# Optimization experiments

Hardware: AMD Instinct MI355X
Metric: run time of the kernel (lower is better)

The kernel has to match this reference:

```python
import jax, jax.numpy as jnp
import numpy as np

N = 30000
SLOPE = 0.2  # PyG GATConv default negative_slope


def _gat_conv(x, src, dst, W, a_src, a_dst, b, heads, out_ch, concat):
    """PyG GATConv (add_self_loops already applied), eval mode (no dropout).
    x: [N, F_in]; src/dst: [E] int; W: [F_in, heads*out_ch];
    a_src/a_dst: [heads, out_ch]; b: [heads*out_ch] or [out_ch]."""
    n = x.shape[0]
    h = (x @ W).reshape(n, heads, out_ch)              # [N, H, C]
    al_src = jnp.sum(h * a_src, axis=-1)               # [N, H]
    al_dst = jnp.sum(h * a_dst, axis=-1)               # [N, H]
    e = jax.nn.leaky_relu(al_src[src] + al_dst[dst], SLOPE)  # [E, H]
    # segment softmax over incoming edges of each destination node
    m = jax.ops.segment_max(e, dst, num_segments=n)
    ex = jnp.exp(e - m[dst])
    denom = jax.ops.segment_sum(ex, dst, num_segments=n)
    alpha = ex / (denom[dst] + 1e-16)                  # [E, H]
    msg = h[src] * alpha[..., None]                    # [E, H, C]
    out = jax.ops.segment_sum(msg, dst, num_segments=n)  # [N, H, C]
    out = out.reshape(n, heads * out_ch) if concat else out.mean(axis=1)
    return out + b


def setup_inputs() -> dict:
    key = jax.random.key(0)
    ks = jax.random.split(key, 20)
    E = 480000
    IN, H0, H1, LAT = 256, 64, 128, 32
    HEADS = 4
    x = jax.random.normal(ks[0], (N, IN), dtype=jnp.float32)
    edge_index = jax.random.randint(ks[1], (2, E), 0, N, dtype=jnp.int32)

    def gp(k, fin, heads, outc, concat):
        k1, k2, k3, k4 = jax.random.split(k, 4)
        s = 0.1
        W = jax.random.normal(k1, (fin, heads * outc), dtype=jnp.float32) * s
        a_s = jax.random.normal(k2, (heads, outc), dtype=jnp.float32) * s
        a_d = jax.random.normal(k3, (heads, outc), dtype=jnp.float32) * s
        b = jax.random.normal(k4, (heads * outc if concat else outc,), dtype=jnp.float32) * s
        return W, a_s, a_d, b

    W1, as1, ad1, b1 = gp(ks[2], IN, HEADS, H0, True)
    W2, as2, ad2, b2 = gp(ks[3], H0 * HEADS, HEADS, H1, True)
    Wm, asm, adm, bm = gp(ks[4], H1 * HEADS, HEADS, LAT, False)
    Wl, asl, adl, bl = gp(ks[5], H1 * HEADS, HEADS, LAT, False)
    return dict(x=x, edge_index=edge_index,
                W1=W1, as1=as1, ad1=ad1, b1=b1,
                W2=W2, as2=as2, ad2=ad2, b2=b2,
                Wm=Wm, asm=asm, adm=adm, bm=bm,
                Wl=Wl, asl=asl, adl=adl, bl=bl)


def reference(x, edge_index, W1, as1, ad1, b1, W2, as2, ad2, b2,
              Wm, asm, adm, bm, Wl, asl, adl, bl):
    n = x.shape[0]
    # add self loops (PyG GATConv default)
    loop = jnp.arange(n, dtype=edge_index.dtype)
    src = jnp.concatenate([edge_index[0], loop])
    dst = jnp.concatenate([edge_index[1], loop])

    out = _gat_conv(x, src, dst, W1, as1, ad1, b1, heads=4, out_ch=64, concat=True)
    out = jax.nn.relu(out)
    out = _gat_conv(out, src, dst, W2, as2, ad2, b2, heads=4, out_ch=128, concat=True)
    out = jax.nn.relu(out)
    # F.dropout with training=False (eval) is identity
    z_mean = _gat_conv(out, src, dst, Wm, asm, adm, bm, heads=4, out_ch=32, concat=False)
    z_logstd = _gat_conv(out, src, dst, Wl, asl, adl, bl, heads=4, out_ch=32, concat=False)
    return z_mean, z_logstd
```

## Files before the change

### kernel.cpp

```cpp
#include <hip/hip_runtime.h>
#include <cstddef>

typedef __attribute__((ext_vector_type(8))) short short8;
typedef __attribute__((ext_vector_type(4))) float f32x4;
typedef __attribute__((ext_vector_type(8))) _Float16 half8;
typedef __attribute__((ext_vector_type(4))) _Float16 half4;

__device__ __forceinline__ unsigned short f2h(float f) {
    union { _Float16 h; unsigned short u; } x; x.h = (_Float16)f; return x.u;
}
__device__ __forceinline__ float lrelu(float v) { return v > 0.f ? v : 0.2f * v; }


__global__ void count_edges_kernel(const int* __restrict__ ei, int E, int N,
                                   int* __restrict__ cnt) {
    int e = blockIdx.x * blockDim.x + threadIdx.x;
    if (e >= E + N) return;
    int d = (e < E) ? ei[E + e] : (e - E);
    atomicAdd(&cnt[d], 1);
}

__global__ void scan_kernel(int* __restrict__ cnt, int* __restrict__ rp, int n) {
    __shared__ int sh[1024];
    int t = threadIdx.x;
    int chunk = (n + 1023) >> 10;
    int beg = t * chunk;
    int end = beg + chunk < n ? beg + chunk : n;
    int local = 0;
    for (int i = beg; i < end; i++) local += cnt[i];
    sh[t] = local;
    __syncthreads();
    for (int off = 1; off < 1024; off <<= 1) {
        int v = (t >= off) ? sh[t - off] : 0;
        __syncthreads();
        sh[t] += v;
        __syncthreads();
    }
    int run = (t == 0) ? 0 : sh[t - 1];
    for (int i = beg; i < end; i++) {
        int c = cnt[i];
        cnt[i] = 0;
        run += c;
        rp[i + 1] = run;
    }
    if (t == 0) rp[0] = 0;
}

__global__ void scatter_edges_kernel(const int* __restrict__ ei, int E, int N,
                                     const int* __restrict__ rp, int* __restrict__ cur,
                                     int* __restrict__ csrc) {
    int e = blockIdx.x * blockDim.x + threadIdx.x;
    if (e >= E + N) return;
    int s, d;
    if (e < E) { s = ei[e]; d = ei[E + e]; } else { s = e - E; d = s; }
    int pos = rp[d] + atomicAdd(&cur[d], 1);
    csrc[pos] = s;
}


__global__ void f32_to_f16_pad4_kernel(const float* __restrict__ in,
                                       unsigned short* __restrict__ out,
                                       int rows, int cols, int padRows) {
    int i = blockIdx.x * blockDim.x + threadIdx.x;
    int total = (padRows * cols) >> 2;
    if (i >= total) return;
    int r = (i * 4) / cols;
    ushort4 o;
    if (r < rows) {
        float4 v = *(const float4*)(in + (size_t)i * 4);
        o = make_ushort4(f2h(v.x), f2h(v.y), f2h(v.z), f2h(v.w));
    } else {
        o = make_ushort4(0, 0, 0, 0);
    }
    *(ushort4*)(out + (size_t)i * 4) = o;
}

__global__ void transpose_all_kernel(
    const float* __restrict__ W1, const float* __restrict__ W2,
    const float* __restrict__ Wm, const float* __restrict__ Wl,
    unsigned short* __restrict__ W1t, unsigned short* __restrict__ W2t,
    unsigned short* __restrict__ WmlT) {
    int i = blockIdx.x * blockDim.x + threadIdx.x;
    if (i < 65536) {
        int k = i >> 8, n = i & 255;
        W1t[(size_t)n * 256 + k] = f2h(W1[i]);
    } else if (i < 65536 + 131072) {
        int j = i - 65536;
        int k = j >> 9, n = j & 511;
        W2t[(size_t)n * 256 + k] = f2h(W2[j]);
    } else if (i < 65536 + 131072 + 65536) {
        int j = i - 196608;
        int k = j >> 7, n = j & 127;
        WmlT[(size_t)n * 512 + k] = f2h(Wm[j]);
    } else if (i < 65536 + 131072 + 131072) {
        int j = i - 262144;
        int k = j >> 7, n = j & 127;
        WmlT[(size_t)(128 + n) * 512 + k] = f2h(Wl[j]);
    }
}


__global__ __launch_bounds__(256) void gemm_f16_kernel(
    const unsigned short* __restrict__ A, const unsigned short* __restrict__ Bt,
    unsigned short* __restrict__ C, int M, int K, int Nc,
    float* __restrict__ al_s, float* __restrict__ al_d,
    const float* __restrict__ aslo, const float* __restrict__ adlo,
    const float* __restrict__ ashi, const float* __restrict__ adhi,
    int csplit, int Chead, int H) {
    __shared__ short As[64 * 32];
    __shared__ short Bs[128 * 32];
    __shared__ float salS[64][4];
    __shared__ float salD[64][4];
    int tid = threadIdx.x;
    int bm = blockIdx.y * 64;
    int bn = blockIdx.x * 128;
    int wave = tid >> 6, lane = tid & 63;
    int wm = (wave >> 1) * 32, wn = (wave & 1) * 64;
    int lm = lane & 15, lq = lane >> 4;

    f32x4 acc[2][4] = {};

    int c0 = tid, c1 = tid + 256;
    const unsigned short* Ap0 = A + (size_t)(bm + (c0 >> 2)) * K + (c0 & 3) * 8;
    const unsigned short* Bp0 = Bt + (size_t)(bn + (c0 >> 2)) * K + (c0 & 3) * 8;
    const unsigned short* Bp1 = Bt + (size_t)(bn + (c1 >> 2)) * K + (c1 & 3) * 8;

    short8 a0 = *(const short8*)(Ap0);
    short8 b0 = *(const short8*)(Bp0);
    short8 b1 = *(const short8*)(Bp1);

    for (int kk = 0; kk < K; kk += 32) {
        __syncthreads();
        *(short8*)&As[c0 * 8] = a0;
        *(short8*)&Bs[c0 * 8] = b0;
        *(short8*)&Bs[c1 * 8] = b1;
        if (kk + 32 < K) {
            a0 = *(const short8*)(Ap0 + kk + 32);
            b0 = *(const short8*)(Bp0 + kk + 32);
            b1 = *(const short8*)(Bp1 + kk + 32);
        }
        __syncthreads();
        half8 af[2], bf[4];
#pragma unroll
        for (int t = 0; t < 2; t++)
            af[t] = *(const half8*)&As[(wm + t * 16 + lm) * 32 + lq * 8];
#pragma unroll
        for (int t = 0; t < 4; t++)
            bf[t] = *(const half8*)&Bs[(wn + t * 16 + lm) * 32 + lq * 8];
#pragma unroll
        for (int tm = 0; tm < 2; tm++)
#pragma unroll
            for (int tn = 0; tn < 4; tn++)
                acc[tm][tn] = __builtin_amdgcn_mfma_f32_16x16x32_f16(
                    af[tm], bf[tn], acc[tm][tn], 0, 0, 0);
    }

#pragma unroll
    for (int tm = 0; tm < 2; tm++) {
#pragma unroll
        for (int r = 0; r < 4; r++) {
            int row = bm + wm + tm * 16 + lq * 4 + r;
            if (row < M) {
#pragma unroll
                for (int tn = 0; tn < 4; tn++) {
                    int col = bn + wn + tn * 16 + lm;
                    C[(size_t)row * Nc + col] = f2h(acc[tm][tn][r]);
                }
            }
        }
    }

    float asv[4], adv[4];
#pragma unroll
    for (int tn = 0; tn < 4; tn++) {
        int col = bn + wn + tn * 16 + lm;
        bool hi = col >= csplit;
        int cc = hi ? col - csplit : col;
        asv[tn] = hi ? ashi[cc] : aslo[cc];
        adv[tn] = hi ? adhi[cc] : adlo[cc];
    }
    int gb = wn >> 5;
#pragma unroll
    for (int tm = 0; tm < 2; tm++) {
#pragma unroll
        for (int r = 0; r < 4; r++) {
#pragma unroll
            for (int p = 0; p < 2; p++) {
                float s1 = acc[tm][2 * p][r] * asv[2 * p]
                         + acc[tm][2 * p + 1][r] * asv[2 * p + 1];
                float s2 = acc[tm][2 * p][r] * adv[2 * p]
                         + acc[tm][2 * p + 1][r] * adv[2 * p + 1];
#pragma unroll
                for (int off = 8; off >= 1; off >>= 1) {
                    s1 += __shfl_xor(s1, off);
                    s2 += __shfl_xor(s2, off);
                }
                if (lm == 0) {
                    int rl = wm + tm * 16 + lq * 4 + r;
                    salS[rl][gb + p] = s1;
                    salD[rl][gb + p] = s2;
                }
            }
        }
    }
    __syncthreads();
    if (tid < 64) {
        int row = bm + tid;
        if (row < M) {
            int hb = bn / Chead;
            int HB = 128 / Chead;
            int GH = Chead >> 5;
            for (int i = 0; i < HB; i++) {
                float ss = 0.f, sd = 0.f;
                for (int j = 0; j < GH; j++) {
                    ss += salS[tid][i * GH + j];
                    sd += salD[tid][i * GH + j];
                }
                al_s[(size_t)row * H + hb + i] = ss;
                al_d[(size_t)row * H + hb + i] = sd;
            }
        }
    }
}


template <int H4, int V, int MODE>
__global__ __launch_bounds__(256) void gat_fused_kernel(
    const int* __restrict__ rp, const int* __restrict__ csrc,
    const float* __restrict__ al_s, const float* __restrict__ al_d,
    const unsigned short* __restrict__ h,
    const float* __restrict__ bias1, const float* __restrict__ bias2,
    void* __restrict__ out1v, void* __restrict__ out2v, int HC, int C, int N) {
    const int H = 4 * H4;
    __shared__ int lds_src[4][64];
    __shared__ float lds_alpha[4][64 * 4 * H4];
    __shared__ float shred[4][256];
    int wv = threadIdx.x >> 6;
    int lane = threadIdx.x & 63;
    int n = blockIdx.x * 4 + wv;
    if (n >= N) return;
    int beg = rp[n], end = rp[n + 1];
    int deg = end - beg;

    float ad[H];
#pragma unroll
    for (int g = 0; g < H4; g++)
        *(float4*)&ad[g * 4] = *(const float4*)(al_d + (size_t)n * H + g * 4);

    int ch = lane * V;
    int hh = ch / C;
    half8 acc8 = {};
    half4 acc4 = {};

    if (deg <= 64) {
        bool act = lane < deg;
        int s = act ? csrc[beg + lane] : 0;
        float v[H], m[H], ex[H], sum[H];
#pragma unroll
        for (int g = 0; g < H4; g++) {
            float4 as = *(const float4*)(al_s + (size_t)s * H + g * 4);
            v[g * 4 + 0] = lrelu(as.x + ad[g * 4 + 0]);
            v[g * 4 + 1] = lrelu(as.y + ad[g * 4 + 1]);
            v[g * 4 + 2] = lrelu(as.z + ad[g * 4 + 2]);
            v[g * 4 + 3] = lrelu(as.w + ad[g * 4 + 3]);
        }
#pragma unroll
        for (int j = 0; j < H; j++) m[j] = act ? v[j] : -3.402823466e38f;
#pragma unroll
        for (int off = 32; off >= 1; off >>= 1)
#pragma unroll
            for (int j = 0; j < H; j++) m[j] = fmaxf(m[j], __shfl_xor(m[j], off));
#pragma unroll
        for (int j = 0; j < H; j++) {
            ex[j] = act ? __expf(v[j] - m[j]) : 0.f;
            sum[j] = ex[j];
        }
#pragma unroll
        for (int off = 32; off >= 1; off >>= 1)
#pragma unroll
            for (int j = 0; j < H; j++) sum[j] += __shfl_xor(sum[j], off);
        if (act) {
            lds_src[wv][lane] = s;
#pragma unroll
            for (int g = 0; g < H4; g++) {
                float4 o;
                o.x = ex[g * 4 + 0] / (sum[g * 4 + 0] + 1e-16f);
                o.y = ex[g * 4 + 1] / (sum[g * 4 + 1] + 1e-16f);
                o.z = ex[g * 4 + 2] / (sum[g * 4 + 2] + 1e-16f);
                o.w = ex[g * 4 + 3] / (sum[g * 4 + 3] + 1e-16f);
                *(float4*)&lds_alpha[wv][lane * H + g * 4] = o;
            }
        }
        int t = 0;
        for (; t + 8 <= deg; t += 8) {
            int ss[8]; float av[8];
#pragma unroll
            for (int u = 0; u < 8; u++) {
                ss[u] = lds_src[wv][t + u];
                av[u] = lds_alpha[wv][(t + u) * H + hh];
            }
            if constexpr (V == 8) {
                half8 hv[8];
#pragma unroll
                for (int u = 0; u < 8; u++)
                    hv[u] = *(const half8*)(h + (size_t)ss[u] * HC + ch);
#pragma unroll
                for (int u = 0; u < 8; u++) {
                    _Float16 ah = (_Float16)av[u];
                    half8 a2;
#pragma unroll
                    for (int i = 0; i < 8; i++) a2[i] = ah;
                    acc8 += hv[u] * a2;
                }
            } else {
                half4 hv[8];
#pragma unroll
                for (int u = 0; u < 8; u++)
                    hv[u] = *(const half4*)(h + (size_t)ss[u] * HC + ch);
#pragma unroll
                for (int u = 0; u < 8; u++) {
                    _Float16 ah = (_Float16)av[u];
                    half4 a2;
#pragma unroll
                    for (int i = 0; i < 4; i++) a2[i] = ah;
                    acc4 += hv[u] * a2;
                }
            }
        }
        for (; t < deg; t++) {
            int s2 = lds_src[wv][t];
            _Float16 ah = (_Float16)lds_alpha[wv][t * H + hh];
            if constexpr (V == 8) {
                half8 hv = *(const half8*)(h + (size_t)s2 * HC + ch);
                half8 a2;
#pragma unroll
                for (int i = 0; i < 8; i++) a2[i] = ah;
                acc8 += hv * a2;
            } else {
                half4 hv = *(const half4*)(h + (size_t)s2 * HC + ch);
                half4 a2;
#pragma unroll
                for (int i = 0; i < 4; i++) a2[i] = ah;
                acc4 += hv * a2;
            }
        }
    } else {
        float m[H], sum[H];
#pragma unroll
        for (int j = 0; j < H; j++) m[j] = -3.402823466e38f;
        for (int e = beg + lane; e < end; e += 64) {
            int s = csrc[e];
#pragma unroll
            for (int g = 0; g < H4; g++) {
                float4 as = *(const float4*)(al_s + (size_t)s * H + g * 4);
                m[g * 4 + 0] = fmaxf(m[g * 4 + 0], lrelu(as.x + ad[g * 4 + 0]));
                m[g * 4 + 1] = fmaxf(m[g * 4 + 1], lrelu(as.y + ad[g * 4 + 1]));
                m[g * 4 + 2] = fmaxf(m[g * 4 + 2], lrelu(as.z + ad[g * 4 + 2]));
                m[g * 4 + 3] = fmaxf(m[g * 4 + 3], lrelu(as.w + ad[g * 4 + 3]));
            }
        }
#pragma unroll
        for (int off = 32; off >= 1; off >>= 1)
#pragma unroll
            for (int j = 0; j < H; j++) m[j] = fmaxf(m[j], __shfl_xor(m[j], off));
#pragma unroll
        for (int j = 0; j < H; j++) sum[j] = 0.f;
        for (int e = beg + lane; e < end; e += 64) {
            int s = csrc[e];
#pragma unroll
            for (int g = 0; g < H4; g++) {
                float4 as = *(const float4*)(al_s + (size_t)s * H + g * 4);
                sum[g * 4 + 0] += __expf(lrelu(as.x + ad[g * 4 + 0]) - m[g * 4 + 0]);
                sum[g * 4 + 1] += __expf(lrelu(as.y + ad[g * 4 + 1]) - m[g * 4 + 1]);
                sum[g * 4 + 2] += __expf(lrelu(as.z + ad[g * 4 + 2]) - m[g * 4 + 2]);
                sum[g * 4 + 3] += __expf(lrelu(as.w + ad[g * 4 + 3]) - m[g * 4 + 3]);
            }
        }
#pragma unroll
        for (int off = 32; off >= 1; off >>= 1)
#pragma unroll
            for (int j = 0; j < H; j++) sum[j] += __shfl_xor(sum[j], off);
        float r[H];
#pragma unroll
        for (int j = 0; j < H; j++) r[j] = 1.0f / (sum[j] + 1e-16f);
        for (int base = beg; base < end; base += 64) {
            int cn = end - base < 64 ? end - base : 64;
            if (lane < cn) {
                int s = csrc[base + lane];
                lds_src[wv][lane] = s;
#pragma unroll
                for (int g = 0; g < H4; g++) {
                    float4 as = *(const float4*)(al_s + (size_t)s * H + g * 4);
                    float4 o;
                    o.x = __expf(lrelu(as.x + ad[g * 4 + 0]) - m[g * 4 + 0]) * r[g * 4 + 0];
                    o.y = __expf(lrelu(as.y + ad[g * 4 + 1]) - m[g * 4 + 1]) * r[g * 4 + 1];
                    o.z = __expf(lrelu(as.z + ad[g * 4 + 2]) - m[g * 4 + 2]) * r[g * 4 + 2];
                    o.w = __expf(lrelu(as.w + ad[g * 4 + 3]) - m[g * 4 + 3]) * r[g * 4 + 3];
                    *(float4*)&lds_alpha[wv][lane * H + g * 4] = o;
                }
            }
            for (int t = 0; t < cn; t++) {
                int s2 = lds_src[wv][t];
                _Float16 ah = (_Float16)lds_alpha[wv][t * H + hh];
                if constexpr (V == 8) {
                    half8 hv = *(const half8*)(h + (size_t)s2 * HC + ch);
                    half8 a2;
#pragma unroll
                    for (int i = 0; i < 8; i++) a2[i] = ah;
                    acc8 += hv * a2;
                } else {
                    half4 hv = *(const half4*)(h + (size_t)s2 * HC + ch);
                    half4 a2;
#pragma unroll
                    for (int i = 0; i < 4; i++) a2[i] = ah;
                    acc4 += hv * a2;
                }
            }
        }
    }

    float accf[V];
#pragma unroll
    for (int j = 0; j < V; j++)
        accf[j] = (V == 8) ? (float)acc8[j] : (float)acc4[j];

    if constexpr (MODE == 0) {
        unsigned short* out = (unsigned short*)out1v;
        unsigned short o[V];
#pragma unroll
        for (int j = 0; j < V; j++)
            o[j] = f2h(fmaxf(accf[j] + bias1[ch + j], 0.f));
        if constexpr (V == 8) {
            short8 ov;
#pragma unroll
            for (int j = 0; j < 8; j++) ov[j] = (short)o[j];
            *(short8*)(out + (size_t)n * HC + ch) = ov;
        } else {
            *(ushort4*)(out + (size_t)n * HC + ch) = make_ushort4(o[0], o[1], o[2], o[3]);
        }
    } else {
        *(float4*)&shred[wv][ch] = make_float4(accf[0], accf[1], accf[2], accf[3]);
        if (lane < 32) {
            float v1 = (shred[wv][lane] + shred[wv][lane + 32] + shred[wv][lane + 64]
                        + shred[wv][lane + 96]) * 0.25f + bias1[lane];
            float v2 = (shred[wv][lane + 128] + shred[wv][lane + 160]
                        + shred[wv][lane + 192] + shred[wv][lane + 224]) * 0.25f
                       + bias2[lane];
            ((float*)out1v)[(size_t)n * 32 + lane] = v1;
            ((float*)out2v)[(size_t)n * 32 + lane] = v2;
        }
    }
}


extern "C" void kernel_launch(void* const* d_in, const int* in_sizes, int n_in,
                              void* d_out, int out_size, void* d_ws, size_t ws_size,
                              hipStream_t stream) {
    (void)n_in; (void)out_size; (void)ws_size;
    const float* x   = (const float*)d_in[0];
    const int*   ei  = (const int*)d_in[1];
    const float* W1  = (const float*)d_in[2];
    const float* as1 = (const float*)d_in[3];
    const float* ad1 = (const float*)d_in[4];
    const float* b1  = (const float*)d_in[5];
    const float* W2  = (const float*)d_in[6];
    const float* as2 = (const float*)d_in[7];
    const float* ad2 = (const float*)d_in[8];
    const float* b2  = (const float*)d_in[9];
    const float* Wm  = (const float*)d_in[10];
    const float* a_sm = (const float*)d_in[11];
    const float* a_dm = (const float*)d_in[12];
    const float* bm  = (const float*)d_in[13];
    const float* Wl  = (const float*)d_in[14];
    const float* a_sl = (const float*)d_in[15];
    const float* a_dl = (const float*)d_in[16];
    const float* bl  = (const float*)d_in[17];
    float* outp = (float*)d_out;

    const int N  = in_sizes[0] / 256;
    const int E  = in_sizes[1] / 2;
    const int ET = E + N;
    const int gM128 = (N + 127) / 128;
    const int Mp = gM128 * 128;
    const int gM64 = (N + 63) / 64;

    auto align_up = [](size_t v) { return (v + 255) & ~(size_t)255; };
    char* w = (char*)d_ws;
    int* row_ptr = (int*)w;  w += align_up((size_t)(N + 1) * 4);
    int* cnt     = (int*)w;  w += align_up((size_t)N * 4);
    int* csrc    = (int*)w;  w += align_up((size_t)ET * 4);
    float* al_s  = (float*)w; w += align_up((size_t)N * 8 * 4);
    float* al_d  = (float*)w; w += align_up((size_t)N * 8 * 4);
    unsigned short* xb   = (unsigned short*)w; w += align_up((size_t)Mp * 256 * 2);
    unsigned short* W1t  = (unsigned short*)w; w += align_up((size_t)256 * 256 * 2);
    unsigned short* W2t  = (unsigned short*)w; w += align_up((size_t)512 * 256 * 2);
    unsigned short* WmlT = (unsigned short*)w; w += align_up((size_t)256 * 512 * 2);
    unsigned short* bufH = (unsigned short*)w; w += align_up((size_t)Mp * 512 * 2);
    unsigned short* bufO = (unsigned short*)w; w += align_up((size_t)Mp * 512 * 2);

    int gzE = (ET + 255) / 256;
    hipMemsetAsync(cnt, 0, (size_t)N * 4, stream);
    count_edges_kernel<<<gzE, 256, 0, stream>>>(ei, E, N, cnt);
    scan_kernel<<<1, 1024, 0, stream>>>(cnt, row_ptr, N);
    scatter_edges_kernel<<<gzE, 256, 0, stream>>>(ei, E, N, row_ptr, cnt, csrc);

    f32_to_f16_pad4_kernel<<<((Mp * 256 / 4) + 255) / 256, 256, 0, stream>>>(
        x, xb, N, 256, Mp);
    transpose_all_kernel<<<(393216 + 255) / 256, 256, 0, stream>>>(
        W1, W2, Wm, Wl, W1t, W2t, WmlT);

    int gF = (N + 3) / 4;

    gemm_f16_kernel<<<dim3(2, gM64), 256, 0, stream>>>(
        xb, W1t, bufH, N, 256, 256, al_s, al_d, as1, ad1, as1, ad1, 256, 64, 4);
    gat_fused_kernel<1, 4, 0><<<gF, 256, 0, stream>>>(
        row_ptr, csrc, al_s, al_d, bufH, b1, nullptr, bufO, nullptr, 256, 64, N);

    gemm_f16_kernel<<<dim3(4, gM64), 256, 0, stream>>>(
        bufO, W2t, bufH, N, 256, 512, al_s, al_d, as2, ad2, as2, ad2, 512, 128, 4);
    gat_fused_kernel<1, 8, 0><<<gF, 256, 0, stream>>>(
        row_ptr, csrc, al_s, al_d, bufH, b2, nullptr, bufO, nullptr, 512, 128, N);

    gemm_f16_kernel<<<dim3(2, gM64), 256, 0, stream>>>(
        bufO, WmlT, bufH, N, 512, 256, al_s, al_d, a_sm, a_dm, a_sl, a_dl, 128, 32, 8);
    gat_fused_kernel<2, 4, 1><<<gF, 256, 0, stream>>>(
        row_ptr, csrc, al_s, al_d, bufH, bm, bl, outp, outp + (size_t)N * 32, 256, 32, N);
}
```

Before: 443.5 us.

## Split fused GAT kernel into edge-alpha pass and channel-sliced aggregation kernels

Replaces the fused per-node softmax-plus-aggregation kernel with two kernels. The first computes softmax attention coefficients and stores them as fp16 in a head-major edge array, reusing the x staging buffer. The second aggregates with several wavefronts per node, each covering a 64-channel slice, with edge groups spread across lanes and fp32 accumulation reduced by shuffles. The aim is more parallelism and memory-level concurrency in the gather. The cost is an extra launch and a global round-trip for the alpha values per layer.

```diff
diff --git a/kernel.cpp b/kernel.cpp
--- a/kernel.cpp
+++ b/kernel.cpp
@@ -4,10 +4,12 @@
 typedef __attribute__((ext_vector_type(8))) short short8;
 typedef __attribute__((ext_vector_type(4))) float f32x4;
 typedef __attribute__((ext_vector_type(8))) _Float16 half8;
-typedef __attribute__((ext_vector_type(4))) _Float16 half4;
 
 __device__ __forceinline__ unsigned short f2h(float f) {
     union { _Float16 h; unsigned short u; } x; x.h = (_Float16)f; return x.u;
+}
+__device__ __forceinline__ float h2f(unsigned short u) {
+    union { unsigned short u; _Float16 h; } x; x.u = u; return (float)x.h;
 }
 __device__ __forceinline__ float lrelu(float v) { return v > 0.f ? v : 0.2f * v; }
 
@@ -224,17 +226,12 @@
 }
 
 
-template <int H4, int V, int MODE>
-__global__ __launch_bounds__(256) void gat_fused_kernel(
+template <int H4>
+__global__ __launch_bounds__(256) void alpha_kernel(
     const int* __restrict__ rp, const int* __restrict__ csrc,
     const float* __restrict__ al_s, const float* __restrict__ al_d,
-    const unsigned short* __restrict__ h,
-    const float* __restrict__ bias1, const float* __restrict__ bias2,
-    void* __restrict__ out1v, void* __restrict__ out2v, int HC, int C, int N) {
+    unsigned short* __restrict__ alphaT, int Ep, int N) {
     const int H = 4 * H4;
-    __shared__ int lds_src[4][64];
-    __shared__ float lds_alpha[4][64 * 4 * H4];
-    __shared__ float shred[4][256];
     int wv = threadIdx.x >> 6;
     int lane = threadIdx.x & 63;
     int n = blockIdx.x * 4 + wv;
@@ -247,11 +244,6 @@
     for (int g = 0; g < H4; g++)
         *(float4*)&ad[g * 4] = *(const float4*)(al_d + (size_t)n * H + g * 4);
 
-    int ch = lane * V;
-    int hh = ch / C;
-    half8 acc8 = {};
-    half4 acc4 = {};
-
     if (deg <= 64) {
         bool act = lane < deg;
         int s = act ? csrc[beg + lane] : 0;
@@ -280,69 +272,9 @@
 #pragma unroll
             for (int j = 0; j < H; j++) sum[j] += __shfl_xor(sum[j], off);
         if (act) {
-            lds_src[wv][lane] = s;
-#pragma unroll
-            for (int g = 0; g < H4; g++) {
-                float4 o;
-                o.x = ex[g * 4 + 0] / (sum[g * 4 + 0] + 1e-16f);
-                o.y = ex[g * 4 + 1] / (sum[g * 4 + 1] + 1e-16f);
-                o.z = ex[g * 4 + 2] / (sum[g * 4 + 2] + 1e-16f);
-                o.w = ex[g * 4 + 3] / (sum[g * 4 + 3] + 1e-16f);
-                *(float4*)&lds_alpha[wv][lane * H + g * 4] = o;
-            }
-        }
-        int t = 0;
-        for (; t + 8 <= deg; t += 8) {
-            int ss[8]; float av[8];
-#pragma unroll
-            for (int u = 0; u < 8; u++) {
-                ss[u] = lds_src[wv][t + u];
-                av[u] = lds_alpha[wv][(t + u) * H + hh];
-            }
-            if constexpr (V == 8) {
-                half8 hv[8];
-#pragma unroll
-                for (int u = 0; u < 8; u++)
-                    hv[u] = *(const half8*)(h + (size_t)ss[u] * HC + ch);
-#pragma unroll
-                for (int u = 0; u < 8; u++) {
-                    _Float16 ah = (_Float16)av[u];
-                    half8 a2;
-#pragma unroll
-                    for (int i = 0; i < 8; i++) a2[i] = ah;
-                    acc8 += hv[u] * a2;
-                }
-            } else {
-                half4 hv[8];
-#pragma unroll
-                for (int u = 0; u < 8; u++)
-                    hv[u] = *(const half4*)(h + (size_t)ss[u] * HC + ch);
-#pragma unroll
-                for (int u = 0; u < 8; u++) {
-                    _Float16 ah = (_Float16)av[u];
-                    half4 a2;
-#pragma unroll
-                    for (int i = 0; i < 4; i++) a2[i] = ah;
-                    acc4 += hv[u] * a2;
-                }
-            }
-        }
-        for (; t < deg; t++) {
-            int s2 = lds_src[wv][t];
-            _Float16 ah = (_Float16)lds_alpha[wv][t * H + hh];
-            if constexpr (V == 8) {
-                half8 hv = *(const half8*)(h + (size_t)s2 * HC + ch);
-                half8 a2;
-#pragma unroll
-                for (int i = 0; i < 8; i++) a2[i] = ah;
-                acc8 += hv * a2;
-            } else {
-                half4 hv = *(const half4*)(h + (size_t)s2 * HC + ch);
-                half4 a2;
-#pragma unroll
-                for (int i = 0; i < 4; i++) a2[i] = ah;
-                acc4 += hv * a2;
-            }
+#pragma unroll
+            for (int j = 0; j < H; j++)
+                alphaT[(size_t)j * Ep + beg + lane] = f2h(ex[j] / (sum[j] + 1e-16f));
         }
     } else {
         float m[H], sum[H];
@@ -383,72 +315,108 @@
         float r[H];
 #pragma unroll
         for (int j = 0; j < H; j++) r[j] = 1.0f / (sum[j] + 1e-16f);
-        for (int base = beg; base < end; base += 64) {
-            int cn = end - base < 64 ? end - base : 64;
-            if (lane < cn) {
-                int s = csrc[base + lane];
-                lds_src[wv][lane] = s;
-#pragma unroll
-                for (int g = 0; g < H4; g++) {
-                    float4 as = *(const float4*)(al_s + (size_t)s * H + g * 4);
-                    float4 o;
-                    o.x = __expf(lrelu(as.x + ad[g * 4 + 0]) - m[g * 4 + 0]) * r[g * 4 + 0];
-                    o.y = __expf(lrelu(as.y + ad[g * 4 + 1]) - m[g * 4 + 1]) * r[g * 4 + 1];
-                    o.z = __expf(lrelu(as.z + ad[g * 4 + 2]) - m[g * 4 + 2]) * r[g * 4 + 2];
-                    o.w = __expf(lrelu(as.w + ad[g * 4 + 3]) - m[g * 4 + 3]) * r[g * 4 + 3];
-                    *(float4*)&lds_alpha[wv][lane * H + g * 4] = o;
-                }
+        for (int e = beg + lane; e < end; e += 64) {
+            int s = csrc[e];
+#pragma unroll
+            for (int g = 0; g < H4; g++) {
+                float4 as = *(const float4*)(al_s + (size_t)s * H + g * 4);
+                alphaT[(size_t)(g * 4 + 0) * Ep + e] =
+                    f2h(__expf(lrelu(as.x + ad[g * 4 + 0]) - m[g * 4 + 0]) * r[g * 4 + 0]);
+                alphaT[(size_t)(g * 4 + 1) * Ep + e] =
+                    f2h(__expf(lrelu(as.y + ad[g * 4 + 1]) - m[g * 4 + 1]) * r[g * 4 + 1]);
+                alphaT[(size_t)(g * 4 + 2) * Ep + e] =
+                    f2h(__expf(lrelu(as.z + ad[g * 4 + 2]) - m[g * 4 + 2]) * r[g * 4 + 2]);
+                alphaT[(size_t)(g * 4 + 3) * Ep + e] =
+                    f2h(__expf(lrelu(as.w + ad[g * 4 + 3]) - m[g * 4 + 3]) * r[g * 4 + 3]);
             }
-            for (int t = 0; t < cn; t++) {
-                int s2 = lds_src[wv][t];
-                _Float16 ah = (_Float16)lds_alpha[wv][t * H + hh];
-                if constexpr (V == 8) {
-                    half8 hv = *(const half8*)(h + (size_t)s2 * HC + ch);
-                    half8 a2;
-#pragma unroll
-                    for (int i = 0; i < 8; i++) a2[i] = ah;
-                    acc8 += hv * a2;
-                } else {
-                    half4 hv = *(const half4*)(h + (size_t)s2 * HC + ch);
-                    half4 a2;
-#pragma unroll
-                    for (int i = 0; i < 4; i++) a2[i] = ah;
-                    acc4 += hv * a2;
-                }
-            }
-        }
-    }
-
-    float accf[V];
-#pragma unroll
-    for (int j = 0; j < V; j++)
-        accf[j] = (V == 8) ? (float)acc8[j] : (float)acc4[j];
-
-    if constexpr (MODE == 0) {
-        unsigned short* out = (unsigned short*)out1v;
-        unsigned short o[V];
-#pragma unroll
-        for (int j = 0; j < V; j++)
-            o[j] = f2h(fmaxf(accf[j] + bias1[ch + j], 0.f));
-        if constexpr (V == 8) {
-            short8 ov;
-#pragma unroll
-            for (int j = 0; j < 8; j++) ov[j] = (short)o[j];
-            *(short8*)(out + (size_t)n * HC + ch) = ov;
-        } else {
-            *(ushort4*)(out + (size_t)n * HC + ch) = make_ushort4(o[0], o[1], o[2], o[3]);
-        }
-    } else {
-        *(float4*)&shred[wv][ch] = make_float4(accf[0], accf[1], accf[2], accf[3]);
-        if (lane < 32) {
-            float v1 = (shred[wv][lane] + shred[wv][lane + 32] + shred[wv][lane + 64]
-                        + shred[wv][lane + 96]) * 0.25f + bias1[lane];
-            float v2 = (shred[wv][lane + 128] + shred[wv][lane + 160]
-                        + shred[wv][lane + 192] + shred[wv][lane + 224]) * 0.25f
-                       + bias2[lane];
-            ((float*)out1v)[(size_t)n * 32 + lane] = v1;
-            ((float*)out2v)[(size_t)n * 32 + lane] = v2;
-        }
+        }
+    }
+}
+
+
+template <int NS, int HC, int C>
+__global__ __launch_bounds__(256) void agg_concat_kernel(
+    const int* __restrict__ rp, const int* __restrict__ csrc,
+    const unsigned short* __restrict__ alphaT, int Ep,
+    const unsigned short* __restrict__ h, const float* __restrict__ bias,
+    unsigned short* __restrict__ out, int N) {
+    int wv = threadIdx.x >> 6;
+    int lane = threadIdx.x & 63;
+    int bs = blockIdx.x % NS;
+    int n = (blockIdx.x / NS) * 4 + wv;
+    if (n >= N) return;
+    int beg = rp[n], end = rp[n + 1];
+    int eg = lane >> 3;
+    int cg = lane & 7;
+    int ch = bs * 64 + cg * 8;
+    const unsigned short* at = alphaT + (size_t)((bs * 64) / C) * Ep;
+    const unsigned short* hp = h + ch;
+    float acc[8] = {};
+    for (int t = beg + eg; t < end; t += 8) {
+        int s = csrc[t];
+        float a = h2f(at[t]);
+        half8 hv = *(const half8*)(hp + (size_t)s * HC);
+#pragma unroll
+        for (int i = 0; i < 8; i++) acc[i] += a * (float)hv[i];
+    }
+#pragma unroll
+    for (int off = 8; off <= 32; off <<= 1)
+#pragma unroll
+        for (int i = 0; i < 8; i++) acc[i] += __shfl_xor(acc[i], off);
+    if (eg == 0) {
+        short8 o;
+#pragma unroll
+        for (int i = 0; i < 8; i++)
+            o[i] = (short)f2h(fmaxf(acc[i] + bias[ch + i], 0.f));
+        *(short8*)(out + (size_t)n * HC + ch) = o;
+    }
+}
+
+
+__global__ __launch_bounds__(256) void agg_mean_kernel(
+    const int* __restrict__ rp, const int* __restrict__ csrc,
+    const unsigned short* __restrict__ alphaT, int Ep,
+    const unsigned short* __restrict__ h,
+    const float* __restrict__ bias1, const float* __restrict__ bias2,
+    float* __restrict__ out1, float* __restrict__ out2, int N) {
+    int wv = threadIdx.x >> 6;
+    int lane = threadIdx.x & 63;
+    int o = blockIdx.x & 1;
+    int n = (blockIdx.x >> 1) * 4 + wv;
+    if (n >= N) return;
+    int beg = rp[n], end = rp[n + 1];
+    int eg = lane >> 4;
+    int cg = lane & 15;
+    int ch = o * 128 + cg * 8;
+    const unsigned short* at = alphaT + (size_t)(o * 4 + (cg >> 2)) * Ep;
+    const unsigned short* hp = h + ch;
+    float acc[8] = {};
+    for (int t = beg + eg; t < end; t += 4) {
+        int s = csrc[t];
+        float a = h2f(at[t]);
+        half8 hv = *(const half8*)(hp + (size_t)s * 256);
+#pragma unroll
+        for (int i = 0; i < 8; i++) acc[i] += a * (float)hv[i];
+    }
+#pragma unroll
+    for (int off = 4; off <= 32; off <<= 1)
+#pragma unroll
+        for (int i = 0; i < 8; i++) acc[i] += __shfl_xor(acc[i], off);
+    if (lane < 4) {
+        const float* bb = o ? bias2 : bias1;
+        float* op = o ? out2 : out1;
+        int wc = lane * 8;
+        float4 r0, r1;
+        r0.x = acc[0] * 0.25f + bb[wc + 0];
+        r0.y = acc[1] * 0.25f + bb[wc + 1];
+        r0.z = acc[2] * 0.25f + bb[wc + 2];
+        r0.w = acc[3] * 0.25f + bb[wc + 3];
+        r1.x = acc[4] * 0.25f + bb[wc + 4];
+        r1.y = acc[5] * 0.25f + bb[wc + 5];
+        r1.z = acc[6] * 0.25f + bb[wc + 6];
+        r1.w = acc[7] * 0.25f + bb[wc + 7];
+        *(float4*)(op + (size_t)n * 32 + wc) = r0;
+        *(float4*)(op + (size_t)n * 32 + wc + 4) = r1;
     }
 }
 
@@ -497,6 +465,7 @@
     unsigned short* WmlT = (unsigned short*)w; w += align_up((size_t)256 * 512 * 2);
     unsigned short* bufH = (unsigned short*)w; w += align_up((size_t)Mp * 512 * 2);
     unsigned short* bufO = (unsigned short*)w; w += align_up((size_t)Mp * 512 * 2);
+    unsigned short* alphaT = xb;
 
     int gzE = (ET + 255) / 256;
     hipMemsetAsync(cnt, 0, (size_t)N * 4, stream);
@@ -513,16 +482,19 @@
 
     gemm_f16_kernel<<<dim3(2, gM64), 256, 0, stream>>>(
         xb, W1t, bufH, N, 256, 256, al_s, al_d, as1, ad1, as1, ad1, 256, 64, 4);
-    gat_fused_kernel<1, 4, 0><<<gF, 256, 0, stream>>>(
-        row_ptr, csrc, al_s, al_d, bufH, b1, nullptr, bufO, nullptr, 256, 64, N);
+    alpha_kernel<1><<<gF, 256, 0, stream>>>(row_ptr, csrc, al_s, al_d, alphaT, ET, N);
+    agg_concat_kernel<4, 256, 64><<<4 * gF, 256, 0, stream>>>(
+        row_ptr, csrc, alphaT, ET, bufH, b1, bufO, N);
 
     gemm_f16_kernel<<<dim3(4, gM64), 256, 0, stream>>>(
         bufO, W2t, bufH, N, 256, 512, al_s, al_d, as2, ad2, as2, ad2, 512, 128, 4);
-    gat_fused_kernel<1, 8, 0><<<gF, 256, 0, stream>>>(
-        row_ptr, csrc, al_s, al_d, bufH, b2, nullptr, bufO, nullptr, 512, 128, N);
+    alpha_kernel<1><<<gF, 256, 0, stream>>>(row_ptr, csrc, al_s, al_d, alphaT, ET, N);
+    agg_concat_kernel<8, 512, 128><<<8 * gF, 256, 0, stream>>>(
+        row_ptr, csrc, alphaT, ET, bufH, b2, bufO, N);
 
     gemm_f16_kernel<<<dim3(2, gM64), 256, 0, stream>>>(
         bufO, WmlT, bufH, N, 512, 256, al_s, al_d, a_sm, a_dm, a_sl, a_dl, 128, 32, 8);
-    gat_fused_kernel<2, 4, 1><<<gF, 256, 0, stream>>>(
-        row_ptr, csrc, al_s, al_d, bufH, bm, bl, outp, outp + (size_t)N * 32, 256, 32, N);
-}
+    alpha_kernel<2><<<gF, 256, 0, stream>>>(row_ptr, csrc, al_s, al_d, alphaT, ET, N);
+    agg_mean_kernel<<<2 * gF, 256, 0, stream>>>(
+        row_ptr, csrc, alphaT, ET, bufH, bm, bl, outp, outp + (size_t)N * 32, N);
+}
```

Measured after the change: 549.0 us. 23.8% more time.
